# Optimization experiments

Hardware: AMD Instinct MI355X
Metric: run time of the kernel (lower is better)

Reference implementation:

```python
import jax, jax.numpy as jnp
import numpy as np

ROPE_BASE = 10000.0

def _rope_cos_sin(T, dh, dtype):
    inv_freq = 1.0 / (ROPE_BASE ** (jnp.arange(0, dh, 2, dtype=jnp.float32) / dh))
    t = jnp.arange(T, dtype=jnp.float32)
    freqs = jnp.outer(t, inv_freq)                      # [T, dh/2]
    emb = jnp.concatenate([freqs, freqs], axis=-1)      # [T, dh]
    return jnp.cos(emb).astype(dtype), jnp.sin(emb).astype(dtype)

def _rotate_half(x):
    x1, x2 = jnp.split(x, 2, axis=-1)
    return jnp.concatenate([-x2, x1], axis=-1)

def setup_inputs() -> dict:
    key = jax.random.key(0)
    k1, k2, k3 = jax.random.split(key, 3)
    B, T, D = 2, 2048, 2048
    x = jax.random.normal(k1, (B, T, D), dtype=jnp.float32)
    w_qkv = jax.random.normal(k2, (3 * D, D), dtype=jnp.float32) * (D ** -0.5)
    w_proj = jax.random.normal(k3, (D, D), dtype=jnp.float32) * (D ** -0.5)
    return {"x": x, "w_qkv": w_qkv, "w_proj": w_proj}

def reference(x, w_qkv, w_proj):
    B, T, D = x.shape
    H = 16
    Dh = D // H
    scale = Dh ** -0.5
    qkv = x @ w_qkv.T                                   # [B,T,3D]
    qkv = qkv.reshape(B, T, 3, H, Dh).transpose(2, 0, 3, 1, 4)  # [3,B,H,T,Dh]
    q, k, v = qkv[0], qkv[1], qkv[2]
    cos, sin = _rope_cos_sin(T, Dh, x.dtype)            # [T,Dh] each, offset=0
    q = q * cos + _rotate_half(q) * sin
    k = k * cos + _rotate_half(k) * sin
    attn = jnp.einsum('bhqd,bhkd->bhqk', q, k) * scale  # [B,H,T,T]
    causal = jnp.triu(jnp.full((T, T), -jnp.inf, dtype=attn.dtype), k=1)
    attn = jax.nn.softmax(attn + causal, axis=-1)
    out = jnp.einsum('bhqk,bhkd->bhqd', attn, v)        # [B,H,T,Dh]
    out = out.transpose(0, 2, 1, 3).reshape(B, T, D)
    return out @ w_proj.T
```

## Files before the change

### kernel.cpp

```cpp
#include <hip/hip_runtime.h>
#include <stdint.h>

typedef unsigned short u16;
typedef unsigned int   u32;
typedef __attribute__((ext_vector_type(8))) __bf16 bf16x8;
typedef __attribute__((ext_vector_type(4))) float  f32x4;

#define MFMA_16x16x32_BF16(a, b, c) __builtin_amdgcn_mfma_f32_16x16x32_bf16((a), (b), (c), 0, 0, 0)

__device__ __forceinline__ u16 f2b(float f) {
    u32 u = __builtin_bit_cast(u32, f);
    u32 r = (u + 0x7FFFu + ((u >> 16) & 1u)) >> 16;
    return (u16)r;
}
__device__ __forceinline__ float b2f(u16 h) {
    u32 u = ((u32)h) << 16;
    return __builtin_bit_cast(float, u);
}

__device__ __forceinline__ void gload_lds16(const void* g, void* l) {
    __builtin_amdgcn_global_load_lds(
        (const __attribute__((address_space(1))) u32*)g,
        (__attribute__((address_space(3))) u32*)l,
        16, 0, 0);
}

__global__ __launch_bounds__(256) void cast3(const float* __restrict__ x,
                                             const float* __restrict__ wq,
                                             const float* __restrict__ wp,
                                             u16* __restrict__ xb,
                                             u16* __restrict__ wqb,
                                             u16* __restrict__ wpb) {
    const int n1 = 8388608, n2 = 12582912, n3 = 4194304;
    const int total4 = (n1 + n2 + n3) / 4;
    for (int i = blockIdx.x * blockDim.x + threadIdx.x; i < total4;
         i += gridDim.x * blockDim.x) {
        int e = i * 4;
        const float* src; u16* dst; int off;
        if (e < n1)            { src = x;  dst = xb;  off = e; }
        else if (e < n1 + n2)  { src = wq; dst = wqb; off = e - n1; }
        else                   { src = wp; dst = wpb; off = e - n1 - n2; }
        float4 v = *(const float4*)(src + off);
        ushort4 o;
        o.x = f2b(v.x); o.y = f2b(v.y); o.z = f2b(v.z); o.w = f2b(v.w);
        *(ushort4*)(dst + off) = o;
    }
}

template <int OUT_BF16>
__global__ __launch_bounds__(256) void gemm_bt(const u16* __restrict__ A,
                                               const u16* __restrict__ Bt,
                                               void* __restrict__ Cout,
                                               int M, int N, int K) {
    __shared__ u16 Al[128 * 64];
    __shared__ u16 Bl[128 * 64];
    const int tid  = threadIdx.x;
    const int w    = tid >> 6;
    const int lane = tid & 63;
    const int quad = lane >> 4;
    const int l16  = lane & 15;
    const int m0 = blockIdx.y * 128;
    const int n0 = blockIdx.x * 128;
    const int wm = (w >> 1) * 64;
    const int wn = (w & 1) * 64;

    f32x4 acc[4][4];
#pragma unroll
    for (int i = 0; i < 4; i++) {
#pragma unroll
        for (int j = 0; j < 4; j++) acc[i][j] = (f32x4){0.f, 0.f, 0.f, 0.f};
    }

    const int srow = tid >> 3;
    const int scol = ((tid & 7) ^ (srow & 7)) * 8;
    const u16* Abase = A + (size_t)(m0 + srow) * K + scol;
    const u16* Bbase = Bt + (size_t)(n0 + srow) * K + scol;
    char* AlB = (char*)Al + w * 1024;
    char* BlB = (char*)Bl + w * 1024;
    const int fx = (l16 & 7);

    for (int k0 = 0; k0 < K; k0 += 64) {
        __syncthreads();
#pragma unroll
        for (int i = 0; i < 4; i++) {
            gload_lds16(Abase + (size_t)i * 32 * K + k0, AlB + i * 4096);
            gload_lds16(Bbase + (size_t)i * 32 * K + k0, BlB + i * 4096);
        }
        __syncthreads();
#pragma unroll
        for (int ks = 0; ks < 2; ks++) {
            const int cb = ((ks * 4 + quad) ^ fx) * 8;
            bf16x8 Af[4];
#pragma unroll
            for (int mi = 0; mi < 4; mi++)
                Af[mi] = *(const bf16x8*)&Al[(wm + mi * 16 + l16) * 64 + cb];
#pragma unroll
            for (int ni = 0; ni < 4; ni++) {
                bf16x8 Bf = *(const bf16x8*)&Bl[(wn + ni * 16 + l16) * 64 + cb];
#pragma unroll
                for (int mi = 0; mi < 4; mi++)
                    acc[mi][ni] = MFMA_16x16x32_BF16(Af[mi], Bf, acc[mi][ni]);
            }
        }
    }

    const int row0 = m0 + wm + quad * 4;
    const int col0 = n0 + wn + l16;
#pragma unroll
    for (int mi = 0; mi < 4; mi++) {
#pragma unroll
        for (int r = 0; r < 4; r++) {
            size_t rowb = (size_t)(row0 + mi * 16 + r) * N;
#pragma unroll
            for (int ni = 0; ni < 4; ni++) {
                float v = acc[mi][ni][r];
                if (OUT_BF16) ((u16*)Cout)[rowb + col0 + ni * 16] = f2b(v);
                else          ((float*)Cout)[rowb + col0 + ni * 16] = v;
            }
        }
    }
}

__global__ __launch_bounds__(256) void rope_qk(const u16* __restrict__ qkv,
                                               u16* __restrict__ Q,
                                               u16* __restrict__ K) {
    __shared__ float cs[64], sn[64];
    const int bt = blockIdx.x;
    const int b = bt >> 11, t = bt & 2047;
    const u16* row = qkv + (size_t)bt * 6144;
    const int tid = threadIdx.x;

    if (tid < 64) {
        float inv = __expf(-0.14391156f * (float)tid);
        float s, c;
        sincosf((float)t * inv, &s, &c);
        sn[tid] = s; cs[tid] = c;
    }
    __syncthreads();

    const int qk = tid >> 7;
    const int h  = (tid >> 3) & 15;
    const int i0 = (tid & 7) * 8;
    const u16* src = row + qk * 2048 + h * 128;
    uint4 a  = *(const uint4*)(src + i0);
    uint4 b4 = *(const uint4*)(src + i0 + 64);
    const u16* pa = (const u16*)&a;
    const u16* pb = (const u16*)&b4;
    u16 o1[8], o2[8];
#pragma unroll
    for (int j = 0; j < 8; j++) {
        int i = i0 + j;
        float x1 = b2f(pa[j]), x2 = b2f(pb[j]);
        float s = sn[i], c = cs[i];
        o1[j] = f2b(x1 * c - x2 * s);
        o2[j] = f2b(x2 * c + x1 * s);
    }
    u16* dst = (qk ? K : Q) + ((size_t)((b * 16 + h) * 2048 + t)) * 128;
    *(uint4*)(dst + i0)      = *(uint4*)o1;
    *(uint4*)(dst + i0 + 64) = *(uint4*)o2;
}

__global__ __launch_bounds__(256) void vtrans(const u16* __restrict__ qkv,
                                              u16* __restrict__ VT) {
    __shared__ u16 S[64 * 136];
    const int tc = blockIdx.x;
    const int bh = blockIdx.y;
    const int b = bh >> 4, h = bh & 15;
    const int tid = threadIdx.x;

#pragma unroll
    for (int i = 0; i < 4; i++) {
        int idx = i * 256 + tid;
        int t  = idx >> 4;
        int d8 = (idx & 15) * 8;
        uint4 v = *(const uint4*)(qkv + ((size_t)(b * 2048 + tc * 64 + t)) * 6144
                                      + 4096 + h * 128 + d8);
        *(uint4*)&S[t * 136 + d8] = v;
    }
    __syncthreads();
#pragma unroll
    for (int i = 0; i < 4; i++) {
        int idx = i * 256 + tid;
        int d  = idx >> 3;
        int t8 = (idx & 7) * 8;
        u16 tmp[8];
#pragma unroll
        for (int j = 0; j < 8; j++) tmp[j] = S[(t8 + j) * 136 + d];
        *(uint4*)(VT + ((size_t)(bh * 128 + d)) * 2048 + tc * 64 + t8) = *(uint4*)tmp;
    }
}

__global__ __launch_bounds__(256) void attn(const u16* __restrict__ Q,
                                            const u16* __restrict__ Kg,
                                            const u16* __restrict__ VTg,
                                            u16* __restrict__ O) {
    __shared__ u16 Kl[2][64 * 128];
    __shared__ u16 Vt[2][128 * 64];
    __shared__ u16 Pl[4 * 16 * 76];

    const int tid  = threadIdx.x;
    const int w    = tid >> 6;
    const int lane = tid & 63;
    const int quad = lane >> 4;
    const int l16  = lane & 15;
    const int pair = blockIdx.x;
    const int bh   = blockIdx.y;
    const int b = bh >> 4, h = bh & 15;
    const size_t base = (size_t)bh * 2048 * 128;
    const u16* Qb  = Q + base;
    const u16* Kb  = Kg + base;
    const u16* VTb = VTg + base;
    u16* Plw = Pl + w * 16 * 76;
    const float scale = 0.08838834764831845f;

    const int krow = tid >> 4;
    const int kcol = (((tid & 15) ^ (krow & 7)) * 8);
    const int vrow = w * 8 + (lane >> 3);
    const int vcol = (((lane & 7) ^ (vrow & 7)) * 8);
    const int fx   = (l16 & 7);

    for (int s = 0; s < 2; s++) {
        const int qt   = s ? (31 - pair) : pair;
        const int q0   = qt * 64;
        const int row0 = q0 + w * 16;

        bf16x8 Qf[4];
#pragma unroll
        for (int kk = 0; kk < 4; kk++)
            Qf[kk] = *(const bf16x8*)&Qb[(size_t)(row0 + l16) * 128 + kk * 32 + quad * 8];

        f32x4 Oacc[8];
#pragma unroll
        for (int ni = 0; ni < 8; ni++) Oacc[ni] = (f32x4){0.f, 0.f, 0.f, 0.f};
        float mrow = -1e30f, lrow = 0.f;

        const int nkt = qt + 1;

        __syncthreads();
        {
            const u16* ksrc = Kb + (size_t)krow * 128 + kcol;
            char* kdst = (char*)Kl[0] + w * 1024;
            const u16* vsrc = VTb + (size_t)vrow * 2048 + vcol;
            char* vdst = (char*)Vt[0] + w * 1024;
#pragma unroll
            for (int i = 0; i < 4; i++) {
                gload_lds16(ksrc + (size_t)i * 16 * 128, kdst + i * 4096);
                gload_lds16(vsrc + (size_t)i * 32 * 2048, vdst + i * 4096);
            }
        }

        for (int kt = 0; kt < nkt; kt++) {
            const int kt0 = kt * 64;
            const int cur = kt & 1;
            __syncthreads();

            if (kt + 1 < nkt) {
                const int kt1 = kt0 + 64;
                const u16* ksrc = Kb + (size_t)(kt1 + krow) * 128 + kcol;
                char* kdst = (char*)Kl[cur ^ 1] + w * 1024;
                const u16* vsrc = VTb + (size_t)vrow * 2048 + kt1 + vcol;
                char* vdst = (char*)Vt[cur ^ 1] + w * 1024;
#pragma unroll
                for (int i = 0; i < 4; i++) {
                    gload_lds16(ksrc + (size_t)i * 16 * 128, kdst + i * 4096);
                    gload_lds16(vsrc + (size_t)i * 32 * 2048, vdst + i * 4096);
                }
            }

            const u16* Klc = Kl[cur];
            const u16* Vtc = Vt[cur];

            f32x4 ST[4];
#pragma unroll
            for (int mi = 0; mi < 4; mi++) ST[mi] = (f32x4){0.f, 0.f, 0.f, 0.f};
#pragma unroll
            for (int kk = 0; kk < 4; kk++) {
                const int cb = ((kk * 4 + quad) ^ fx) * 8;
#pragma unroll
                for (int mi = 0; mi < 4; mi++) {
                    bf16x8 Kf = *(const bf16x8*)&Klc[(mi * 16 + l16) * 128 + cb];
                    ST[mi] = MFMA_16x16x32_BF16(Kf, Qf[kk], ST[mi]);
                }
            }

            const bool needs_mask = (kt0 + 63) > row0;
            const int qg = row0 + l16;
            float tmax = -1e30f;
#pragma unroll
            for (int mi = 0; mi < 4; mi++) {
#pragma unroll
                for (int r = 0; r < 4; r++) {
                    float sv = ST[mi][r] * scale;
                    if (needs_mask) {
                        int kg = kt0 + mi * 16 + quad * 4 + r;
                        sv = (kg > qg) ? -1e30f : sv;
                    }
                    ST[mi][r] = sv;
                    tmax = fmaxf(tmax, sv);
                }
            }
            tmax = fmaxf(tmax, __shfl_xor(tmax, 16));
            tmax = fmaxf(tmax, __shfl_xor(tmax, 32));

            if (__any(tmax > mrow + 8.0f)) {
                float mnew  = fmaxf(mrow, tmax);
                float alpha = __expf(mrow - mnew);
                mrow = mnew;
                lrow *= alpha;
                float aRow[4];
#pragma unroll
                for (int r = 0; r < 4; r++) aRow[r] = __shfl(alpha, quad * 4 + r);
#pragma unroll
                for (int ni = 0; ni < 8; ni++) {
#pragma unroll
                    for (int r = 0; r < 4; r++) Oacc[ni][r] *= aRow[r];
                }
            }

            float tsum = 0.f;
#pragma unroll
            for (int mi = 0; mi < 4; mi++) {
#pragma unroll
                for (int r = 0; r < 4; r++) {
                    float p = __expf(ST[mi][r] - mrow);
                    ST[mi][r] = p;
                    tsum += p;
                }
            }
            lrow += tsum;

#pragma unroll
            for (int mi = 0; mi < 4; mi++) {
                ushort4 pk;
                pk.x = f2b(ST[mi][0]); pk.y = f2b(ST[mi][1]);
                pk.z = f2b(ST[mi][2]); pk.w = f2b(ST[mi][3]);
                *(ushort4*)&Plw[l16 * 76 + mi * 16 + quad * 4] = pk;
            }

            bf16x8 Pf[2];
#pragma unroll
            for (int kk = 0; kk < 2; kk++)
                Pf[kk] = *(const bf16x8*)&Plw[l16 * 76 + kk * 32 + quad * 8];
#pragma unroll
            for (int kk = 0; kk < 2; kk++) {
                const int cb = ((kk * 4 + quad) ^ fx) * 8;
#pragma unroll
                for (int ni = 0; ni < 8; ni++) {
                    bf16x8 Vf = *(const bf16x8*)&Vtc[(ni * 16 + l16) * 64 + cb];
                    Oacc[ni] = MFMA_16x16x32_BF16(Pf[kk], Vf, Oacc[ni]);
                }
            }
        }

        lrow += __shfl_xor(lrow, 16);
        lrow += __shfl_xor(lrow, 32);
        float inv = 1.0f / lrow;
        float iRow[4];
#pragma unroll
        for (int r = 0; r < 4; r++) iRow[r] = __shfl(inv, quad * 4 + r);

#pragma unroll
        for (int r = 0; r < 4; r++) {
            int t = row0 + quad * 4 + r;
            size_t rowb = ((size_t)(b * 2048 + t)) * 2048 + (size_t)(h * 128);
#pragma unroll
            for (int ni = 0; ni < 8; ni++)
                O[rowb + ni * 16 + l16] = f2b(Oacc[ni][r] * iRow[r]);
        }
    }
}

extern "C" void kernel_launch(void* const* d_in, const int* in_sizes, int n_in,
                              void* d_out, int out_size, void* d_ws, size_t ws_size,
                              hipStream_t stream) {
    const float* x  = (const float*)d_in[0];
    const float* wq = (const float*)d_in[1];
    const float* wp = (const float*)d_in[2];

    char* ws = (char*)d_ws;
    u16* xb   = (u16*)(ws + 0);
    u16* wqb  = (u16*)(ws + 16777216);
    u16* wpb  = (u16*)(ws + 41943040);
    u16* qkvb = (u16*)(ws + 50331648);
    u16* Qr   = (u16*)(ws + 100663296);
    u16* Kr   = (u16*)(ws + 117440512);
    u16* VTt  = (u16*)(ws + 134217728);
    u16* Ob   = (u16*)(ws + 50331648);
    if (ws_size < 150994944) return;

    cast3<<<2048, 256, 0, stream>>>(x, wq, wp, xb, wqb, wpb);
    gemm_bt<1><<<dim3(48, 32), 256, 0, stream>>>(xb, wqb, qkvb, 4096, 6144, 2048);
    rope_qk<<<4096, 256, 0, stream>>>(qkvb, Qr, Kr);
    vtrans<<<dim3(32, 32), 256, 0, stream>>>(qkvb, VTt);
    attn<<<dim3(16, 32), 256, 0, stream>>>(Qr, Kr, VTt, Ob);
    gemm_bt<0><<<dim3(16, 32), 256, 0, stream>>>(Ob, wpb, (float*)d_out, 4096, 2048, 2048);
}
```

Measured before the change: 396.1 us.

## Shrink attention tiles to 32 rows with 2-wave blocks and more blocks

Reworks the flash-attention kernel to use 32-row query tiles and 32-key KV tiles, run by 128-thread blocks (2 waves), and doubles the grid. LDS staging, swizzle patterns and the P·V MFMA loop are adjusted to the smaller tile width. The aim is more blocks, better occupancy and finer causal load balancing. The cost is more K/V reloads per query row, because each loaded K/V tile now serves fewer query rows, plus more barriers per unit of work.

```diff
diff --git a/kernel.cpp b/kernel.cpp
--- a/kernel.cpp
+++ b/kernel.cpp
@@ -190,38 +190,39 @@
     }
 }
 
-__global__ __launch_bounds__(256) void attn(const u16* __restrict__ Q,
-                                            const u16* __restrict__ Kg,
-                                            const u16* __restrict__ VTg,
-                                            u16* __restrict__ O) {
-    __shared__ u16 Kl[2][64 * 128];
-    __shared__ u16 Vt[2][128 * 64];
-    __shared__ u16 Pl[4 * 16 * 76];
+__global__ __launch_bounds__(128, 2) void attn(const u16* __restrict__ Q,
+                                               const u16* __restrict__ Kg,
+                                               const u16* __restrict__ VTg,
+                                               u16* __restrict__ O) {
+    __shared__ u16 Kl[2][32 * 128];
+    __shared__ u16 Vt[2][128 * 32];
+    __shared__ u16 Pl[2 * 16 * 40];
 
     const int tid  = threadIdx.x;
     const int w    = tid >> 6;
     const int lane = tid & 63;
     const int quad = lane >> 4;
     const int l16  = lane & 15;
-    const int pair = blockIdx.x;
+    const int p    = blockIdx.x;
     const int bh   = blockIdx.y;
     const int b = bh >> 4, h = bh & 15;
     const size_t base = (size_t)bh * 2048 * 128;
     const u16* Qb  = Q + base;
     const u16* Kb  = Kg + base;
     const u16* VTb = VTg + base;
-    u16* Plw = Pl + w * 16 * 76;
+    u16* Plw = Pl + w * 16 * 40;
     const float scale = 0.08838834764831845f;
 
     const int krow = tid >> 4;
     const int kcol = (((tid & 15) ^ (krow & 7)) * 8);
-    const int vrow = w * 8 + (lane >> 3);
-    const int vcol = (((lane & 7) ^ (vrow & 7)) * 8);
+    const int vrow = tid >> 2;
+    const int vcol = (((tid & 3) ^ ((vrow >> 1) & 3)) * 8);
     const int fx   = (l16 & 7);
+    const int px   = ((l16 >> 1) & 3);
 
     for (int s = 0; s < 2; s++) {
-        const int qt   = s ? (31 - pair) : pair;
-        const int q0   = qt * 64;
+        const int qt   = s ? (63 - p) : p;
+        const int q0   = qt * 32;
         const int row0 = q0 + w * 16;
 
         bf16x8 Qf[4];
@@ -244,50 +245,50 @@
             char* vdst = (char*)Vt[0] + w * 1024;
 #pragma unroll
             for (int i = 0; i < 4; i++) {
-                gload_lds16(ksrc + (size_t)i * 16 * 128, kdst + i * 4096);
-                gload_lds16(vsrc + (size_t)i * 32 * 2048, vdst + i * 4096);
+                gload_lds16(ksrc + (size_t)i * 8 * 128, kdst + i * 2048);
+                gload_lds16(vsrc + (size_t)i * 32 * 2048, vdst + i * 2048);
             }
         }
 
         for (int kt = 0; kt < nkt; kt++) {
-            const int kt0 = kt * 64;
+            const int kt0 = kt * 32;
             const int cur = kt & 1;
             __syncthreads();
 
             if (kt + 1 < nkt) {
-                const int kt1 = kt0 + 64;
+                const int kt1 = kt0 + 32;
                 const u16* ksrc = Kb + (size_t)(kt1 + krow) * 128 + kcol;
                 char* kdst = (char*)Kl[cur ^ 1] + w * 1024;
                 const u16* vsrc = VTb + (size_t)vrow * 2048 + kt1 + vcol;
                 char* vdst = (char*)Vt[cur ^ 1] + w * 1024;
 #pragma unroll
                 for (int i = 0; i < 4; i++) {
-                    gload_lds16(ksrc + (size_t)i * 16 * 128, kdst + i * 4096);
-                    gload_lds16(vsrc + (size_t)i * 32 * 2048, vdst + i * 4096);
+                    gload_lds16(ksrc + (size_t)i * 8 * 128, kdst + i * 2048);
+                    gload_lds16(vsrc + (size_t)i * 32 * 2048, vdst + i * 2048);
                 }
             }
 
             const u16* Klc = Kl[cur];
             const u16* Vtc = Vt[cur];
 
-            f32x4 ST[4];
-#pragma unroll
-            for (int mi = 0; mi < 4; mi++) ST[mi] = (f32x4){0.f, 0.f, 0.f, 0.f};
+            f32x4 ST[2];
+#pragma unroll
+            for (int mi = 0; mi < 2; mi++) ST[mi] = (f32x4){0.f, 0.f, 0.f, 0.f};
 #pragma unroll
             for (int kk = 0; kk < 4; kk++) {
                 const int cb = ((kk * 4 + quad) ^ fx) * 8;
 #pragma unroll
-                for (int mi = 0; mi < 4; mi++) {
+                for (int mi = 0; mi < 2; mi++) {
                     bf16x8 Kf = *(const bf16x8*)&Klc[(mi * 16 + l16) * 128 + cb];
                     ST[mi] = MFMA_16x16x32_BF16(Kf, Qf[kk], ST[mi]);
                 }
             }
 
-            const bool needs_mask = (kt0 + 63) > row0;
+            const bool needs_mask = (kt0 + 31) > row0;
             const int qg = row0 + l16;
             float tmax = -1e30f;
 #pragma unroll
-            for (int mi = 0; mi < 4; mi++) {
+            for (int mi = 0; mi < 2; mi++) {
 #pragma unroll
                 for (int r = 0; r < 4; r++) {
                     float sv = ST[mi][r] * scale;
@@ -319,36 +320,29 @@
 
             float tsum = 0.f;
 #pragma unroll
-            for (int mi = 0; mi < 4; mi++) {
+            for (int mi = 0; mi < 2; mi++) {
 #pragma unroll
                 for (int r = 0; r < 4; r++) {
-                    float p = __expf(ST[mi][r] - mrow);
-                    ST[mi][r] = p;
-                    tsum += p;
+                    float p2 = __expf(ST[mi][r] - mrow);
+                    ST[mi][r] = p2;
+                    tsum += p2;
                 }
             }
             lrow += tsum;
 
 #pragma unroll
-            for (int mi = 0; mi < 4; mi++) {
+            for (int mi = 0; mi < 2; mi++) {
                 ushort4 pk;
                 pk.x = f2b(ST[mi][0]); pk.y = f2b(ST[mi][1]);
                 pk.z = f2b(ST[mi][2]); pk.w = f2b(ST[mi][3]);
-                *(ushort4*)&Plw[l16 * 76 + mi * 16 + quad * 4] = pk;
-            }
-
-            bf16x8 Pf[2];
-#pragma unroll
-            for (int kk = 0; kk < 2; kk++)
-                Pf[kk] = *(const bf16x8*)&Plw[l16 * 76 + kk * 32 + quad * 8];
-#pragma unroll
-            for (int kk = 0; kk < 2; kk++) {
-                const int cb = ((kk * 4 + quad) ^ fx) * 8;
-#pragma unroll
-                for (int ni = 0; ni < 8; ni++) {
-                    bf16x8 Vf = *(const bf16x8*)&Vtc[(ni * 16 + l16) * 64 + cb];
-                    Oacc[ni] = MFMA_16x16x32_BF16(Pf[kk], Vf, Oacc[ni]);
-                }
+                *(ushort4*)&Plw[l16 * 40 + mi * 16 + quad * 4] = pk;
+            }
+
+            bf16x8 Pf = *(const bf16x8*)&Plw[l16 * 40 + quad * 8];
+#pragma unroll
+            for (int ni = 0; ni < 8; ni++) {
+                bf16x8 Vf = *(const bf16x8*)&Vtc[(ni * 16 + l16) * 32 + (quad ^ px) * 8];
+                Oacc[ni] = MFMA_16x16x32_BF16(Pf, Vf, Oacc[ni]);
             }
         }
 
@@ -392,6 +386,6 @@
     gemm_bt<1><<<dim3(48, 32), 256, 0, stream>>>(xb, wqb, qkvb, 4096, 6144, 2048);
     rope_qk<<<4096, 256, 0, stream>>>(qkvb, Qr, Kr);
     vtrans<<<dim3(32, 32), 256, 0, stream>>>(qkvb, VTt);
-    attn<<<dim3(16, 32), 256, 0, stream>>>(Qr, Kr, VTt, Ob);
+    attn<<<dim3(32, 32), 128, 0, stream>>>(Qr, Kr, VTt, Ob);
     gemm_bt<0><<<dim3(16, 32), 256, 0, stream>>>(Ob, wpb, (float*)d_out, 4096, 2048, 2048);
 }
```

Result: slower. 447.5 us (+13.0%).
